# Optimization experiments

Measured on AMD Instinct MI355X. Metric: run time of the kernel, lower is better.

## Reference

```python
import jax, jax.numpy as jnp
import numpy as np

B, T, I, H = 64, 512, 256, 512


def setup_inputs() -> dict:
    key = jax.random.key(0)
    ks = jax.random.split(key, 3)
    x = jax.random.normal(ks[0], (B, T, I), dtype=jnp.float32)
    W = 0.1 * jax.random.normal(ks[1], (I, H), dtype=jnp.float32)
    U = 0.1 * jax.random.normal(ks[2], (H, H), dtype=jnp.float32)
    bias = jnp.ones((1, H), dtype=jnp.float32)
    alpha = jnp.full((1, 1), -3.0, dtype=jnp.float32)
    beta = jnp.full((1, 1), 3.0, dtype=jnp.float32)
    return {"x": x, "W": W, "U": U, "bias": bias, "alpha": alpha, "beta": beta}


def reference(x, W, U, bias, alpha, beta):
    # FastRNN: h_t = sigmoid(beta)*h_{t-1} + sigmoid(alpha)*tanh(W x_t + U h_{t-1} + b)
    sa = jax.nn.sigmoid(alpha)  # [1,1]
    sb = jax.nn.sigmoid(beta)   # [1,1]
    # Precompute input projection for all timesteps: [B,T,H]
    wx = jnp.einsum('bti,ih->bth', x, W)
    h0 = jnp.zeros((x.shape[0], U.shape[0]), dtype=x.dtype)

    def step(h, wx_t):
        pre = wx_t + h @ U + bias
        c = jnp.tanh(pre)
        h_new = sb * h + sa * c
        return h_new, h_new

    # scan over time: move T to leading axis
    _, hs = jax.lax.scan(step, h0, jnp.swapaxes(wx, 0, 1))
    return jnp.swapaxes(hs, 0, 1)  # [B,T,H]
```

## Files before the change

kernel.cpp:

```cpp
#include <hip/hip_runtime.h>
#include <stdint.h>


#define B_ 64
#define T_ 512
#define I_ 256
#define H_ 512
#define M_ (B_ * T_)

#define WXB_BYTES  ((size_t)M_ * H_ * 4)
#define HHALF_BYTES ((size_t)B_ * H_ * 2)

typedef short v8s __attribute__((ext_vector_type(8)));
typedef float v4f __attribute__((ext_vector_type(4)));
typedef unsigned long long u64t;

__device__ __forceinline__ uint16_t f2bf(float x) {
    union { float f; uint32_t u; } v; v.f = x;
    return (uint16_t)((v.u + 0x7FFFu + ((v.u >> 16) & 1u)) >> 16);
}

__global__ __launch_bounds__(256) void wx_gemm(
        const float* __restrict__ x, const float* __restrict__ W,
        const float* __restrict__ bias, float* __restrict__ wxb) {
    __shared__ uint16_t Asl[64][40];
    __shared__ uint16_t Bsl[4 * 64 * 8];

    const int tid = threadIdx.x;
    const int lane = tid & 63;
    const int w = tid >> 6;
    const int q = lane >> 4, c = lane & 15;
    const int mbase = (int)(blockIdx.x >> 3) * 64;
    const int nbase = (int)(blockIdx.x & 7) * 64;

    v4f acc[4];
    #pragma unroll
    for (int i = 0; i < 4; ++i) acc[i] = (v4f){0.f, 0.f, 0.f, 0.f};

    for (int ks = 0; ks < I_; ks += 32) {
        {
            int row = tid >> 2, c4 = tid & 3;
            const float* gp = x + (size_t)(mbase + row) * I_ + ks + c4 * 8;
            float4 f0 = *(const float4*)gp;
            float4 f1 = *(const float4*)(gp + 4);
            uint16_t* dp = &Asl[row][c4 * 8];
            dp[0] = f2bf(f0.x); dp[1] = f2bf(f0.y); dp[2] = f2bf(f0.z); dp[3] = f2bf(f0.w);
            dp[4] = f2bf(f1.x); dp[5] = f2bf(f1.y); dp[6] = f2bf(f1.z); dp[7] = f2bf(f1.w);
        }
        {
            int nt = tid >> 6;
            const float* gp = W + (size_t)(ks + q * 8) * H_ + nbase + nt * 16 + c;
            union { v8s v; uint16_t u[8]; } pk;
            #pragma unroll
            for (int jj = 0; jj < 8; ++jj) pk.u[jj] = f2bf(gp[(size_t)jj * H_]);
            *(v8s*)&Bsl[(nt * 64 + lane) * 8] = pk.v;
        }
        __syncthreads();
        const v8s* Bf = (const v8s*)Bsl;
        v8s a = *(const v8s*)&Asl[w * 16 + c][q * 8];
        #pragma unroll
        for (int nt = 0; nt < 4; ++nt) {
            v8s b = Bf[nt * 64 + lane];
            acc[nt] = __builtin_amdgcn_mfma_f32_16x16x32_bf16(a, b, acc[nt], 0, 0, 0);
        }
        __syncthreads();
    }
    #pragma unroll
    for (int nt = 0; nt < 4; ++nt) {
        int j = nbase + nt * 16 + c;
        float bj = bias[j];
        #pragma unroll
        for (int r = 0; r < 4; ++r) {
            int m = mbase + w * 16 + q * 4 + r;
            wxb[(size_t)m * H_ + j] = acc[nt][r] + bj;
        }
    }
}

__global__ __launch_bounds__(256, 1) void rnn_scan(
        const float* __restrict__ U, const float* __restrict__ wxb,
        const float* __restrict__ alpha, const float* __restrict__ beta,
        float* __restrict__ out, uint16_t* __restrict__ Hbuf) {
    __shared__ uint16_t Als[2][16][520];
    __shared__ uint16_t Hstg[16][128];

    const int bid = blockIdx.x;
    const int g = bid >> 2, s = bid & 3;
    const int tid = threadIdx.x;
    const int lane = tid & 63;
    const int w = tid >> 6;
    const int q = lane >> 4, c = lane & 15;
    const int row16 = tid >> 4, seg = tid & 15;

    float sa, sb;
    { float a = alpha[0], b = beta[0];
      sa = 1.f / (1.f + __expf(-a)); sb = 1.f / (1.f + __expf(-b)); }

    v8s Uf[2][16];
    #pragma unroll
    for (int nt = 0; nt < 2; ++nt) {
        int jg = s * 128 + (2 * w + nt) * 16 + c;
        #pragma unroll
        for (int kt = 0; kt < 16; ++kt) {
            const float* gp = U + (size_t)(kt * 32 + q * 8) * H_ + jg;
            union { v8s v; uint16_t u[8]; } pk;
            #pragma unroll
            for (int jj = 0; jj < 8; ++jj) pk.u[jj] = f2bf(gp[(size_t)jj * H_]);
            Uf[nt][kt] = pk.v;
        }
    }
    float hold[2][4];
    #pragma unroll
    for (int nt = 0; nt < 2; ++nt)
        #pragma unroll
        for (int r = 0; r < 4; ++r) hold[nt][r] = 0.f;

    float wxv[2][4], wxn[2][4];
    #pragma unroll
    for (int nt = 0; nt < 2; ++nt) {
        int jg = s * 128 + (2 * w + nt) * 16 + c;
        #pragma unroll
        for (int r = 0; r < 4; ++r) {
            int bg = g * 16 + q * 4 + r;
            wxn[nt][r] = __builtin_nontemporal_load(
                &wxb[((size_t)bg * T_ + 0) * H_ + jg]);
        }
    }

    for (int t = 0; t < T_; ++t) {
        const int p = t & 1;
        #pragma unroll
        for (int nt = 0; nt < 2; ++nt)
            #pragma unroll
            for (int r = 0; r < 4; ++r) wxv[nt][r] = wxn[nt][r];
        if (t == 0) {
            uint4 z = {0, 0, 0, 0};
            uint4* dp = (uint4*)((uint16_t*)&Als[0][row16][0] + seg * 32);
            dp[0] = z; dp[1] = z; dp[2] = z; dp[3] = z;
        } else {
            const u64t tau64 = ((t >> 1) & 1) ? 0x0001000100010001ull : 0ull;
            const u64t lsb64 = 0x0001000100010001ull;
            const u64t* gp = (const u64t*)(Hbuf +
                ((size_t)p * B_ + g * 16 + row16) * H_ + seg * 32);
            u64t v[8];
            #pragma unroll
            for (int u2 = 0; u2 < 8; ++u2)
                v[u2] = __hip_atomic_load(&gp[u2], __ATOMIC_RELAXED,
                                          __HIP_MEMORY_SCOPE_AGENT);
            for (int guard = 0; guard < (1 << 20); ++guard) {
                u64t bad = 0;
                #pragma unroll
                for (int u2 = 0; u2 < 8; ++u2)
                    bad |= (v[u2] ^ tau64) & lsb64;
                if (!bad) break;
                #pragma unroll
                for (int u2 = 0; u2 < 8; ++u2)
                    v[u2] = __hip_atomic_load(&gp[u2], __ATOMIC_RELAXED,
                                              __HIP_MEMORY_SCOPE_AGENT);
            }
            u64t* dp = (u64t*)((uint16_t*)&Als[p][row16][0] + seg * 32);
            #pragma unroll
            for (int u2 = 0; u2 < 8; ++u2) dp[u2] = v[u2];
        }
        __syncthreads();
        if (t + 1 < T_) {
            #pragma unroll
            for (int nt = 0; nt < 2; ++nt) {
                int jg = s * 128 + (2 * w + nt) * 16 + c;
                #pragma unroll
                for (int r = 0; r < 4; ++r) {
                    int bg = g * 16 + q * 4 + r;
                    wxn[nt][r] = __builtin_nontemporal_load(
                        &wxb[((size_t)bg * T_ + (t + 1)) * H_ + jg]);
                }
            }
        }
        v4f acc0 = (v4f){0.f, 0.f, 0.f, 0.f};
        v4f acc1 = (v4f){0.f, 0.f, 0.f, 0.f};
        #pragma unroll
        for (int kt = 0; kt < 16; ++kt) {
            v8s a = *(const v8s*)((const uint16_t*)&Als[p][c][0] + kt * 32 + q * 8);
            acc0 = __builtin_amdgcn_mfma_f32_16x16x32_bf16(a, Uf[0][kt], acc0, 0, 0, 0);
            acc1 = __builtin_amdgcn_mfma_f32_16x16x32_bf16(a, Uf[1][kt], acc1, 0, 0, 0);
        }
        const uint16_t tau = (uint16_t)(((t + 1) >> 1) & 1);
        #pragma unroll
        for (int nt = 0; nt < 2; ++nt) {
            v4f av = nt ? acc1 : acc0;
            int jl = (2 * w + nt) * 16 + c;
            #pragma unroll
            for (int r = 0; r < 4; ++r) {
                float pre = av[r] + wxv[nt][r];
                float ex = __expf(pre + pre);
                float ct = 1.f - 2.f * __builtin_amdgcn_rcpf(ex + 1.f);
                float hn = sb * hold[nt][r] + sa * ct;
                hold[nt][r] = hn;
                Hstg[q * 4 + r][jl] = (uint16_t)((f2bf(hn) & 0xFFFEu) | tau);
            }
        }
        __syncthreads();
        {
            int i0 = tid * 2;
            #pragma unroll
            for (int k2 = 0; k2 < 2; ++k2) {
                int i = i0 + k2;
                int b = i >> 5, jo = (i & 31) * 4;
                u64t v = *(const u64t*)&Hstg[b][jo];
                u64t* pp = (u64t*)(Hbuf +
                    ((size_t)(1 - p) * B_ + g * 16 + b) * H_ + s * 128 + jo);
                __hip_atomic_store(pp, v, __ATOMIC_RELAXED,
                                   __HIP_MEMORY_SCOPE_AGENT);
            }
        }
        #pragma unroll
        for (int nt = 0; nt < 2; ++nt) {
            int jg = s * 128 + (2 * w + nt) * 16 + c;
            #pragma unroll
            for (int r = 0; r < 4; ++r) {
                int bg = g * 16 + q * 4 + r;
                out[((size_t)bg * T_ + t) * H_ + jg] = hold[nt][r];
            }
        }
    }
}

extern "C" void kernel_launch(void* const* d_in, const int* in_sizes, int n_in,
                              void* d_out, int out_size, void* d_ws, size_t ws_size,
                              hipStream_t stream) {
    const float* x     = (const float*)d_in[0];
    const float* W     = (const float*)d_in[1];
    const float* U     = (const float*)d_in[2];
    const float* bias  = (const float*)d_in[3];
    const float* alpha = (const float*)d_in[4];
    const float* beta  = (const float*)d_in[5];
    float* out = (float*)d_out;

    char* ws = (char*)d_ws;
    float* wxb = (float*)ws;
    uint16_t* Hbuf = (uint16_t*)(ws + WXB_BYTES);

    hipMemsetAsync(Hbuf, 0x00, HHALF_BYTES, stream);
    hipMemsetAsync((char*)Hbuf + HHALF_BYTES, 0xFF, HHALF_BYTES, stream);

    wx_gemm<<<dim3((M_ / 64) * (H_ / 64)), dim3(256), 0, stream>>>(x, W, bias, wxb);
    rnn_scan<<<dim3(16), dim3(256), 0, stream>>>(U, wxb, alpha, beta, out, Hbuf);
}
```

Before: 1.403 ms.

## Load recurrent hidden state directly into MFMA registers, skipping LDS staging

Each lane now reads the bf16 hidden-state fragments it needs for the MFMA A operand straight from the global exchange buffer into registers, instead of a cooperative load into shared memory followed by LDS reads. The parity-bit readiness check is done on those register fragments, and the loads for the next step are issued speculatively right after this block's stores. The K loop is also split into two accumulator chains to shorten MFMA dependency latency. The aim is to remove an LDS round-trip and overlap the cross-block polling latency, at the cost of many more per-lane global atomic loads, higher register pressure (32 extra u64 values), and redundant loads across waves.

```diff
diff --git a/kernel.cpp b/kernel.cpp
--- a/kernel.cpp
+++ b/kernel.cpp
@@ -81,7 +81,6 @@
         const float* __restrict__ U, const float* __restrict__ wxb,
         const float* __restrict__ alpha, const float* __restrict__ beta,
         float* __restrict__ out, uint16_t* __restrict__ Hbuf) {
-    __shared__ uint16_t Als[2][16][520];
     __shared__ uint16_t Hstg[16][128];
 
     const int bid = blockIdx.x;
@@ -90,7 +89,6 @@
     const int lane = tid & 63;
     const int w = tid >> 6;
     const int q = lane >> 4, c = lane & 15;
-    const int row16 = tid >> 4, seg = tid & 15;
 
     float sa, sb;
     { float a = alpha[0], b = beta[0];
@@ -127,40 +125,45 @@
         }
     }
 
+    const size_t abase = ((size_t)(g * 16 + c) * H_ + q * 8) >> 2;
+
+    u64t av[16][2];
+    #pragma unroll
+    for (int kt = 0; kt < 16; ++kt) { av[kt][0] = 0; av[kt][1] = 0; }
+
     for (int t = 0; t < T_; ++t) {
         const int p = t & 1;
         #pragma unroll
         for (int nt = 0; nt < 2; ++nt)
             #pragma unroll
             for (int r = 0; r < 4; ++r) wxv[nt][r] = wxn[nt][r];
-        if (t == 0) {
-            uint4 z = {0, 0, 0, 0};
-            uint4* dp = (uint4*)((uint16_t*)&Als[0][row16][0] + seg * 32);
-            dp[0] = z; dp[1] = z; dp[2] = z; dp[3] = z;
-        } else {
-            const u64t tau64 = ((t >> 1) & 1) ? 0x0001000100010001ull : 0ull;
-            const u64t lsb64 = 0x0001000100010001ull;
-            const u64t* gp = (const u64t*)(Hbuf +
-                ((size_t)p * B_ + g * 16 + row16) * H_ + seg * 32);
-            u64t v[8];
-            #pragma unroll
-            for (int u2 = 0; u2 < 8; ++u2)
-                v[u2] = __hip_atomic_load(&gp[u2], __ATOMIC_RELAXED,
-                                          __HIP_MEMORY_SCOPE_AGENT);
+
+        if (t > 0) {
+            const u64t* gp = (const u64t*)Hbuf + (size_t)p * (B_ * H_ / 4) + abase;
+            const uint32_t tau = (uint32_t)((t >> 1) & 1);
             for (int guard = 0; guard < (1 << 20); ++guard) {
-                u64t bad = 0;
+                u64t x;
+                if (tau) {
+                    u64t a64 = av[0][0] & av[0][1];
+                    #pragma unroll
+                    for (int kt = 1; kt < 16; ++kt) { a64 &= av[kt][0]; a64 &= av[kt][1]; }
+                    x = ~a64;
+                } else {
+                    u64t o64 = av[0][0] | av[0][1];
+                    #pragma unroll
+                    for (int kt = 1; kt < 16; ++kt) { o64 |= av[kt][0]; o64 |= av[kt][1]; }
+                    x = o64;
+                }
+                uint32_t fold = (uint32_t)(x | (x >> 32));
+                if (!((fold | (fold >> 16)) & 1u)) break;
                 #pragma unroll
-                for (int u2 = 0; u2 < 8; ++u2)
-                    bad |= (v[u2] ^ tau64) & lsb64;
-                if (!bad) break;
-                #pragma unroll
-                for (int u2 = 0; u2 < 8; ++u2)
-                    v[u2] = __hip_atomic_load(&gp[u2], __ATOMIC_RELAXED,
-                                              __HIP_MEMORY_SCOPE_AGENT);
-            }
-            u64t* dp = (u64t*)((uint16_t*)&Als[p][row16][0] + seg * 32);
-            #pragma unroll
-            for (int u2 = 0; u2 < 8; ++u2) dp[u2] = v[u2];
+                for (int kt = 0; kt < 16; ++kt) {
+                    av[kt][0] = __hip_atomic_load(&gp[kt * 8 + 0], __ATOMIC_RELAXED,
+                                                  __HIP_MEMORY_SCOPE_AGENT);
+                    av[kt][1] = __hip_atomic_load(&gp[kt * 8 + 1], __ATOMIC_RELAXED,
+                                                  __HIP_MEMORY_SCOPE_AGENT);
+                }
+            }
         }
         __syncthreads();
         if (t + 1 < T_) {
@@ -175,27 +178,35 @@
                 }
             }
         }
-        v4f acc0 = (v4f){0.f, 0.f, 0.f, 0.f};
-        v4f acc1 = (v4f){0.f, 0.f, 0.f, 0.f};
-        #pragma unroll
-        for (int kt = 0; kt < 16; ++kt) {
-            v8s a = *(const v8s*)((const uint16_t*)&Als[p][c][0] + kt * 32 + q * 8);
-            acc0 = __builtin_amdgcn_mfma_f32_16x16x32_bf16(a, Uf[0][kt], acc0, 0, 0, 0);
-            acc1 = __builtin_amdgcn_mfma_f32_16x16x32_bf16(a, Uf[1][kt], acc1, 0, 0, 0);
-        }
-        const uint16_t tau = (uint16_t)(((t + 1) >> 1) & 1);
+        v4f acc00 = (v4f){0.f, 0.f, 0.f, 0.f};
+        v4f acc01 = (v4f){0.f, 0.f, 0.f, 0.f};
+        v4f acc10 = (v4f){0.f, 0.f, 0.f, 0.f};
+        v4f acc11 = (v4f){0.f, 0.f, 0.f, 0.f};
+        #pragma unroll
+        for (int kt = 0; kt < 16; kt += 2) {
+            union { u64t u[2]; v8s v; } f0, f1;
+            f0.u[0] = av[kt][0];     f0.u[1] = av[kt][1];
+            f1.u[0] = av[kt + 1][0]; f1.u[1] = av[kt + 1][1];
+            acc00 = __builtin_amdgcn_mfma_f32_16x16x32_bf16(f0.v, Uf[0][kt],     acc00, 0, 0, 0);
+            acc10 = __builtin_amdgcn_mfma_f32_16x16x32_bf16(f0.v, Uf[1][kt],     acc10, 0, 0, 0);
+            acc01 = __builtin_amdgcn_mfma_f32_16x16x32_bf16(f1.v, Uf[0][kt + 1], acc01, 0, 0, 0);
+            acc11 = __builtin_amdgcn_mfma_f32_16x16x32_bf16(f1.v, Uf[1][kt + 1], acc11, 0, 0, 0);
+        }
+        v4f accA = acc00 + acc01;
+        v4f accB = acc10 + acc11;
+
+        const uint16_t tauw = (uint16_t)(((t + 1) >> 1) & 1);
         #pragma unroll
         for (int nt = 0; nt < 2; ++nt) {
-            v4f av = nt ? acc1 : acc0;
             int jl = (2 * w + nt) * 16 + c;
             #pragma unroll
             for (int r = 0; r < 4; ++r) {
-                float pre = av[r] + wxv[nt][r];
+                float pre = (nt ? accB[r] : accA[r]) + wxv[nt][r];
                 float ex = __expf(pre + pre);
                 float ct = 1.f - 2.f * __builtin_amdgcn_rcpf(ex + 1.f);
                 float hn = sb * hold[nt][r] + sa * ct;
                 hold[nt][r] = hn;
-                Hstg[q * 4 + r][jl] = (uint16_t)((f2bf(hn) & 0xFFFEu) | tau);
+                Hstg[q * 4 + r][jl] = (uint16_t)((f2bf(hn) & 0xFFFEu) | tauw);
             }
         }
         __syncthreads();
@@ -210,6 +221,16 @@
                     ((size_t)(1 - p) * B_ + g * 16 + b) * H_ + s * 128 + jo);
                 __hip_atomic_store(pp, v, __ATOMIC_RELAXED,
                                    __HIP_MEMORY_SCOPE_AGENT);
+            }
+        }
+        if (t + 1 < T_) {
+            const u64t* gn = (const u64t*)Hbuf + (size_t)(1 - p) * (B_ * H_ / 4) + abase;
+            #pragma unroll
+            for (int kt = 0; kt < 16; ++kt) {
+                av[kt][0] = __hip_atomic_load(&gn[kt * 8 + 0], __ATOMIC_RELAXED,
+                                              __HIP_MEMORY_SCOPE_AGENT);
+                av[kt][1] = __hip_atomic_load(&gn[kt * 8 + 1], __ATOMIC_RELAXED,
+                                              __HIP_MEMORY_SCOPE_AGENT);
             }
         }
         #pragma unroll
```

Result: slower. 3.208 ms (+128.6%).

## Use wide inline-asm polling loads issued early for cross-block hidden-state exchange

Applied to the files above, without the earlier changes.

Replaces the 64-bit relaxed atomic loads and stores used to exchange bf16 hidden state between the four blocks of a group with 128-bit global loads and stores in inline asm carrying sc0 sc1 cache bits. The first poll of the next step's state is issued right after this step's store, so its latency overlaps the loop turnaround, and the parity check reduces whole vectors with AND/OR. The out stores now sit before the staging barrier. The aim is fewer memory instructions and shorter latency on the serial inter-block handoff, at the cost of relying on hand-written memory-coherence semantics and s_waitcnt handling.

```diff
diff --git a/kernel.cpp b/kernel.cpp
--- a/kernel.cpp
+++ b/kernel.cpp
@@ -13,6 +13,7 @@
 
 typedef short v8s __attribute__((ext_vector_type(8)));
 typedef float v4f __attribute__((ext_vector_type(4)));
+typedef unsigned int u32x4 __attribute__((ext_vector_type(4)));
 typedef unsigned long long u64t;
 
 __device__ __forceinline__ uint16_t f2bf(float x) {
@@ -77,12 +78,15 @@
     }
 }
 
+#define POLL_LOAD(qv, ap) \
+    asm volatile("global_load_dwordx4 %0, %1, off sc0 sc1" : "=v"(qv) : "v"(ap))
+
 __global__ __launch_bounds__(256, 1) void rnn_scan(
         const float* __restrict__ U, const float* __restrict__ wxb,
         const float* __restrict__ alpha, const float* __restrict__ beta,
         float* __restrict__ out, uint16_t* __restrict__ Hbuf) {
-    __shared__ uint16_t Als[2][16][520];
-    __shared__ uint16_t Hstg[16][128];
+    __shared__ __align__(16) uint16_t Als[2][16][520];
+    __shared__ __align__(16) uint16_t Hstg[16][128];
 
     const int bid = blockIdx.x;
     const int g = bid >> 2, s = bid & 3;
@@ -90,7 +94,6 @@
     const int lane = tid & 63;
     const int w = tid >> 6;
     const int q = lane >> 4, c = lane & 15;
-    const int row16 = tid >> 4, seg = tid & 15;
 
     float sa, sb;
     { float a = alpha[0], b = beta[0];
@@ -127,40 +130,56 @@
         }
     }
 
+    const size_t rowbase = (size_t)(g * 16) * H_;
+    u32x4 pq0 = {0,0,0,0}, pq1 = {0,0,0,0}, pq2 = {0,0,0,0}, pq3 = {0,0,0,0};
+
     for (int t = 0; t < T_; ++t) {
         const int p = t & 1;
         #pragma unroll
         for (int nt = 0; nt < 2; ++nt)
             #pragma unroll
             for (int r = 0; r < 4; ++r) wxv[nt][r] = wxn[nt][r];
+
         if (t == 0) {
-            uint4 z = {0, 0, 0, 0};
-            uint4* dp = (uint4*)((uint16_t*)&Als[0][row16][0] + seg * 32);
-            dp[0] = z; dp[1] = z; dp[2] = z; dp[3] = z;
+            u32x4 z = {0, 0, 0, 0};
+            #pragma unroll
+            for (int u4 = 0; u4 < 4; ++u4) {
+                int k = tid + 256 * u4;
+                *(u32x4*)&Als[0][k >> 6][(k & 63) * 8] = z;
+            }
         } else {
-            const u64t tau64 = ((t >> 1) & 1) ? 0x0001000100010001ull : 0ull;
-            const u64t lsb64 = 0x0001000100010001ull;
-            const u64t* gp = (const u64t*)(Hbuf +
-                ((size_t)p * B_ + g * 16 + row16) * H_ + seg * 32);
-            u64t v[8];
-            #pragma unroll
-            for (int u2 = 0; u2 < 8; ++u2)
-                v[u2] = __hip_atomic_load(&gp[u2], __ATOMIC_RELAXED,
-                                          __HIP_MEMORY_SCOPE_AGENT);
+            const uint16_t* hb = Hbuf + (size_t)p * (B_ * H_) + rowbase;
+            const uint16_t* a0 = hb + (size_t)(tid + 0)   * 8;
+            const uint16_t* a1 = hb + (size_t)(tid + 256) * 8;
+            const uint16_t* a2 = hb + (size_t)(tid + 512) * 8;
+            const uint16_t* a3 = hb + (size_t)(tid + 768) * 8;
+            const uint32_t tau = (uint32_t)((t >> 1) & 1);
             for (int guard = 0; guard < (1 << 20); ++guard) {
-                u64t bad = 0;
-                #pragma unroll
-                for (int u2 = 0; u2 < 8; ++u2)
-                    bad |= (v[u2] ^ tau64) & lsb64;
-                if (!bad) break;
-                #pragma unroll
-                for (int u2 = 0; u2 < 8; ++u2)
-                    v[u2] = __hip_atomic_load(&gp[u2], __ATOMIC_RELAXED,
-                                              __HIP_MEMORY_SCOPE_AGENT);
-            }
-            u64t* dp = (u64t*)((uint16_t*)&Als[p][row16][0] + seg * 32);
-            #pragma unroll
-            for (int u2 = 0; u2 < 8; ++u2) dp[u2] = v[u2];
+                asm volatile("s_waitcnt vmcnt(0)"
+                             : "+v"(pq0), "+v"(pq1), "+v"(pq2), "+v"(pq3));
+                __builtin_amdgcn_sched_barrier(0);
+                uint32_t bad;
+                if (tau) {
+                    u32x4 av4 = pq0 & pq1 & pq2 & pq3;
+                    bad = ~(av4.x & av4.y & av4.z & av4.w);
+                } else {
+                    u32x4 ov4 = pq0 | pq1 | pq2 | pq3;
+                    bad = ov4.x | ov4.y | ov4.z | ov4.w;
+                }
+                if (!((bad | (bad >> 16)) & 1u)) break;
+                POLL_LOAD(pq0, a0); POLL_LOAD(pq1, a1);
+                POLL_LOAD(pq2, a2); POLL_LOAD(pq3, a3);
+            }
+            {
+                int k0 = tid;
+                *(u32x4*)&Als[p][k0 >> 6][(k0 & 63) * 8] = pq0;
+                int k1 = tid + 256;
+                *(u32x4*)&Als[p][k1 >> 6][(k1 & 63) * 8] = pq1;
+                int k2 = tid + 512;
+                *(u32x4*)&Als[p][k2 >> 6][(k2 & 63) * 8] = pq2;
+                int k3 = tid + 768;
+                *(u32x4*)&Als[p][k3 >> 6][(k3 & 63) * 8] = pq3;
+            }
         }
         __syncthreads();
         if (t + 1 < T_) {
@@ -183,7 +202,7 @@
             acc0 = __builtin_amdgcn_mfma_f32_16x16x32_bf16(a, Uf[0][kt], acc0, 0, 0, 0);
             acc1 = __builtin_amdgcn_mfma_f32_16x16x32_bf16(a, Uf[1][kt], acc1, 0, 0, 0);
         }
-        const uint16_t tau = (uint16_t)(((t + 1) >> 1) & 1);
+        const uint16_t tauw = (uint16_t)(((t + 1) >> 1) & 1);
         #pragma unroll
         for (int nt = 0; nt < 2; ++nt) {
             v4f av = nt ? acc1 : acc0;
@@ -195,21 +214,7 @@
                 float ct = 1.f - 2.f * __builtin_amdgcn_rcpf(ex + 1.f);
                 float hn = sb * hold[nt][r] + sa * ct;
                 hold[nt][r] = hn;
-                Hstg[q * 4 + r][jl] = (uint16_t)((f2bf(hn) & 0xFFFEu) | tau);
-            }
-        }
-        __syncthreads();
-        {
-            int i0 = tid * 2;
-            #pragma unroll
-            for (int k2 = 0; k2 < 2; ++k2) {
-                int i = i0 + k2;
-                int b = i >> 5, jo = (i & 31) * 4;
-                u64t v = *(const u64t*)&Hstg[b][jo];
-                u64t* pp = (u64t*)(Hbuf +
-                    ((size_t)(1 - p) * B_ + g * 16 + b) * H_ + s * 128 + jo);
-                __hip_atomic_store(pp, v, __ATOMIC_RELAXED,
-                                   __HIP_MEMORY_SCOPE_AGENT);
+                Hstg[q * 4 + r][jl] = (uint16_t)((f2bf(hn) & 0xFFFEu) | tauw);
             }
         }
         #pragma unroll
@@ -220,6 +225,24 @@
                 int bg = g * 16 + q * 4 + r;
                 out[((size_t)bg * T_ + t) * H_ + jg] = hold[nt][r];
             }
+        }
+        __syncthreads();
+        {
+            int b = tid >> 4, jo = (tid & 15) * 8;
+            u32x4 val = *(const u32x4*)&Hstg[b][jo];
+            uint16_t* pp = Hbuf +
+                ((size_t)(1 - p) * B_ + g * 16 + b) * H_ + s * 128 + jo;
+            asm volatile("global_store_dwordx4 %0, %1, off sc0 sc1"
+                         :: "v"(pp), "v"(val) : "memory");
+        }
+        if (t + 1 < T_) {
+            const uint16_t* hb = Hbuf + (size_t)(1 - p) * (B_ * H_) + rowbase;
+            const uint16_t* a0 = hb + (size_t)(tid + 0)   * 8;
+            const uint16_t* a1 = hb + (size_t)(tid + 256) * 8;
+            const uint16_t* a2 = hb + (size_t)(tid + 512) * 8;
+            const uint16_t* a3 = hb + (size_t)(tid + 768) * 8;
+            POLL_LOAD(pq0, a0); POLL_LOAD(pq1, a1);
+            POLL_LOAD(pq2, a2); POLL_LOAD(pq3, a3);
         }
     }
 }
```

New measurement: 1.301 ms. -7.2%, faster.

## Split hidden state across two 512-thread blocks per batch group, exchange only remote half

Applied to the files above, without the earlier changes.

Changes the scan partition from four 256-thread blocks per 16-row batch group to two 512-thread blocks, each owning half of the hidden dimension. Each block writes its own new state directly into the LDS operand buffer and only publishes and polls the partner's half through global memory. The first poll is issued right after publishing, so its latency overlaps the output stores. This cuts cross-block flag traffic and spinning per timestep, in exchange for fewer blocks and more per-block register and LDS pressure.

```diff
diff --git a/kernel.cpp b/kernel.cpp
--- a/kernel.cpp
+++ b/kernel.cpp
@@ -77,20 +77,18 @@
     }
 }
 
-__global__ __launch_bounds__(256, 1) void rnn_scan(
+__global__ __launch_bounds__(512, 2) void rnn_scan(
         const float* __restrict__ U, const float* __restrict__ wxb,
         const float* __restrict__ alpha, const float* __restrict__ beta,
         float* __restrict__ out, uint16_t* __restrict__ Hbuf) {
-    __shared__ uint16_t Als[2][16][520];
-    __shared__ uint16_t Hstg[16][128];
+    __shared__ __align__(16) uint16_t Als[2][16][520];
 
     const int bid = blockIdx.x;
-    const int g = bid >> 2, s = bid & 3;
+    const int g = bid >> 1, s = bid & 1;
     const int tid = threadIdx.x;
     const int lane = tid & 63;
     const int w = tid >> 6;
     const int q = lane >> 4, c = lane & 15;
-    const int row16 = tid >> 4, seg = tid & 15;
 
     float sa, sb;
     { float a = alpha[0], b = beta[0];
@@ -99,7 +97,7 @@
     v8s Uf[2][16];
     #pragma unroll
     for (int nt = 0; nt < 2; ++nt) {
-        int jg = s * 128 + (2 * w + nt) * 16 + c;
+        int jg = s * 256 + (2 * w + nt) * 16 + c;
         #pragma unroll
         for (int kt = 0; kt < 16; ++kt) {
             const float* gp = U + (size_t)(kt * 32 + q * 8) * H_ + jg;
@@ -118,7 +116,7 @@
     float wxv[2][4], wxn[2][4];
     #pragma unroll
     for (int nt = 0; nt < 2; ++nt) {
-        int jg = s * 128 + (2 * w + nt) * 16 + c;
+        int jg = s * 256 + (2 * w + nt) * 16 + c;
         #pragma unroll
         for (int r = 0; r < 4; ++r) {
             int bg = g * 16 + q * 4 + r;
@@ -127,46 +125,51 @@
         }
     }
 
+    const int prow = tid >> 5;
+    const int pcol = (1 - s) * 256 + (tid & 31) * 8;
+    const size_t poff = ((size_t)(g * 16 + prow)) * H_ + pcol;
+    const int orow = lane >> 2;
+    const int ocol = s * 256 + w * 32 + (lane & 3) * 8;
+    const size_t ooff = ((size_t)(g * 16 + orow)) * H_ + ocol;
+
+    u64t e0 = 0, e1 = 0;
+
     for (int t = 0; t < T_; ++t) {
         const int p = t & 1;
         #pragma unroll
         for (int nt = 0; nt < 2; ++nt)
             #pragma unroll
             for (int r = 0; r < 4; ++r) wxv[nt][r] = wxn[nt][r];
+
         if (t == 0) {
-            uint4 z = {0, 0, 0, 0};
-            uint4* dp = (uint4*)((uint16_t*)&Als[0][row16][0] + seg * 32);
-            dp[0] = z; dp[1] = z; dp[2] = z; dp[3] = z;
+            u64t z = 0;
+            #pragma unroll
+            for (int u2 = 0; u2 < 4; ++u2) {
+                int k2 = tid * 4 + u2;
+                *((u64t*)&Als[0][k2 >> 7][0] + (k2 & 127)) = z;
+            }
         } else {
-            const u64t tau64 = ((t >> 1) & 1) ? 0x0001000100010001ull : 0ull;
-            const u64t lsb64 = 0x0001000100010001ull;
-            const u64t* gp = (const u64t*)(Hbuf +
-                ((size_t)p * B_ + g * 16 + row16) * H_ + seg * 32);
-            u64t v[8];
-            #pragma unroll
-            for (int u2 = 0; u2 < 8; ++u2)
-                v[u2] = __hip_atomic_load(&gp[u2], __ATOMIC_RELAXED,
-                                          __HIP_MEMORY_SCOPE_AGENT);
+            const u64t* gp = (const u64t*)(Hbuf + (size_t)p * (B_ * H_) + poff);
+            const uint32_t tau = (uint32_t)((t >> 1) & 1);
+            const u64t lsb = 0x0001000100010001ull;
+            const u64t want = tau ? lsb : 0ull;
+            u64t v0 = e0, v1 = e1;
             for (int guard = 0; guard < (1 << 20); ++guard) {
-                u64t bad = 0;
-                #pragma unroll
-                for (int u2 = 0; u2 < 8; ++u2)
-                    bad |= (v[u2] ^ tau64) & lsb64;
-                if (!bad) break;
-                #pragma unroll
-                for (int u2 = 0; u2 < 8; ++u2)
-                    v[u2] = __hip_atomic_load(&gp[u2], __ATOMIC_RELAXED,
-                                              __HIP_MEMORY_SCOPE_AGENT);
-            }
-            u64t* dp = (u64t*)((uint16_t*)&Als[p][row16][0] + seg * 32);
-            #pragma unroll
-            for (int u2 = 0; u2 < 8; ++u2) dp[u2] = v[u2];
+                u64t x = ((v0 ^ want) | (v1 ^ want)) & lsb;
+                if (!x) break;
+                v0 = __hip_atomic_load(&gp[0], __ATOMIC_RELAXED,
+                                       __HIP_MEMORY_SCOPE_AGENT);
+                v1 = __hip_atomic_load(&gp[1], __ATOMIC_RELAXED,
+                                       __HIP_MEMORY_SCOPE_AGENT);
+            }
+            u64t* dp = (u64t*)&Als[p][prow][pcol];
+            dp[0] = v0; dp[1] = v1;
         }
         __syncthreads();
         if (t + 1 < T_) {
             #pragma unroll
             for (int nt = 0; nt < 2; ++nt) {
-                int jg = s * 128 + (2 * w + nt) * 16 + c;
+                int jg = s * 256 + (2 * w + nt) * 16 + c;
                 #pragma unroll
                 for (int r = 0; r < 4; ++r) {
                     int bg = g * 16 + q * 4 + r;
@@ -183,11 +186,11 @@
             acc0 = __builtin_amdgcn_mfma_f32_16x16x32_bf16(a, Uf[0][kt], acc0, 0, 0, 0);
             acc1 = __builtin_amdgcn_mfma_f32_16x16x32_bf16(a, Uf[1][kt], acc1, 0, 0, 0);
         }
-        const uint16_t tau = (uint16_t)(((t + 1) >> 1) & 1);
+        const uint16_t tauw = (uint16_t)(((t + 1) >> 1) & 1);
         #pragma unroll
         for (int nt = 0; nt < 2; ++nt) {
             v4f av = nt ? acc1 : acc0;
-            int jl = (2 * w + nt) * 16 + c;
+            int jl = s * 256 + (2 * w + nt) * 16 + c;
             #pragma unroll
             for (int r = 0; r < 4; ++r) {
                 float pre = av[r] + wxv[nt][r];
@@ -195,26 +198,27 @@
                 float ct = 1.f - 2.f * __builtin_amdgcn_rcpf(ex + 1.f);
                 float hn = sb * hold[nt][r] + sa * ct;
                 hold[nt][r] = hn;
-                Hstg[q * 4 + r][jl] = (uint16_t)((f2bf(hn) & 0xFFFEu) | tau);
-            }
-        }
-        __syncthreads();
-        {
-            int i0 = tid * 2;
-            #pragma unroll
-            for (int k2 = 0; k2 < 2; ++k2) {
-                int i = i0 + k2;
-                int b = i >> 5, jo = (i & 31) * 4;
-                u64t v = *(const u64t*)&Hstg[b][jo];
-                u64t* pp = (u64t*)(Hbuf +
-                    ((size_t)(1 - p) * B_ + g * 16 + b) * H_ + s * 128 + jo);
-                __hip_atomic_store(pp, v, __ATOMIC_RELAXED,
+                Als[1 - p][q * 4 + r][jl] = (uint16_t)((f2bf(hn) & 0xFFFEu) | tauw);
+            }
+        }
+        __syncthreads();
+        if (t + 1 < T_) {
+            const u64t* sp = (const u64t*)&Als[1 - p][orow][ocol];
+            u64t o0 = sp[0], o1 = sp[1];
+            u64t* pp = (u64t*)(Hbuf + (size_t)(1 - p) * (B_ * H_) + ooff);
+            __hip_atomic_store(&pp[0], o0, __ATOMIC_RELAXED,
+                               __HIP_MEMORY_SCOPE_AGENT);
+            __hip_atomic_store(&pp[1], o1, __ATOMIC_RELAXED,
+                               __HIP_MEMORY_SCOPE_AGENT);
+            const u64t* gn = (const u64t*)(Hbuf + (size_t)(1 - p) * (B_ * H_) + poff);
+            e0 = __hip_atomic_load(&gn[0], __ATOMIC_RELAXED,
                                    __HIP_MEMORY_SCOPE_AGENT);
-            }
+            e1 = __hip_atomic_load(&gn[1], __ATOMIC_RELAXED,
+                                   __HIP_MEMORY_SCOPE_AGENT);
         }
         #pragma unroll
         for (int nt = 0; nt < 2; ++nt) {
-            int jg = s * 128 + (2 * w + nt) * 16 + c;
+            int jg = s * 256 + (2 * w + nt) * 16 + c;
             #pragma unroll
             for (int r = 0; r < 4; ++r) {
                 int bg = g * 16 + q * 4 + r;
@@ -243,5 +247,5 @@
     hipMemsetAsync((char*)Hbuf + HHALF_BYTES, 0xFF, HHALF_BYTES, stream);
 
     wx_gemm<<<dim3((M_ / 64) * (H_ / 64)), dim3(256), 0, stream>>>(x, W, bias, wxb);
-    rnn_scan<<<dim3(16), dim3(256), 0, stream>>>(U, wxb, alpha, beta, out, Hbuf);
-}
+    rnn_scan<<<dim3(8), dim3(512), 0, stream>>>(U, wxb, alpha, beta, out, Hbuf);
+}
```

After: 1.630 ms. 1.16x slower.
